# Kernel tuning notes

Measured on AMD Instinct MI355X. Metric: run time of the kernel, lower is better.

## Reference

```python
import jax, jax.numpy as jnp
import numpy as np

MARGIN = 1.0

def _safe_sqrt(x):
    # sqrt with zero gradient at x<=0 (matches relu().sqrt() forward; avoids NaN grads on the zero diagonal)
    pos = x > 0
    return jnp.where(pos, jnp.sqrt(jnp.where(pos, x, 1.0)), 0.0)

def _smoothed_metric_loss(X, m=MARGIN):
    # X: [N, d], N even; lifted-structure smoothed loss (Song et al.)
    N = X.shape[0]
    sq = jnp.sum(X * X, axis=1)                       # [N]
    G = X @ X.T                                       # [N, N]
    D = _safe_sqrt(jax.nn.relu(sq[:, None] + sq[None, :] - 2.0 * G))
    E = jnp.exp(m - D)                                # [N, N]
    P = N // 2
    i = jnp.arange(P) * 2
    j = i + 1
    # negatives for pair p: rows {i,j}, all cols except {i,j}
    row_pair_sum = E.reshape(P, 2, N).sum(axis=(1, 2))  # [P] = rowsum(i)+rowsum(j)
    excl = E[i, i] + E[i, j] + E[j, i] + E[j, j]
    neg_sum = row_pair_sum - excl
    J = jnp.log(neg_sum) + D[i, j]
    return jnp.sum(jax.nn.relu(J) ** 2) / (2.0 * P)

def reference(text_embeddings, shape_embeddings):
    N = text_embeddings.shape[0]
    # tt loss on text embeddings
    metric_tt = _smoothed_metric_loss(text_embeddings, MARGIN)
    # repeat each shape embedding twice (index_select with i//2)
    shape_rep = jnp.repeat(shape_embeddings, 2, axis=0)  # [N, d]
    mask = jnp.tile(jnp.array([1.0, 0.0], dtype=text_embeddings.dtype), N // 2)[:, None]
    inv = 1.0 - mask
    e1 = text_embeddings * mask + shape_rep * inv
    e2 = text_embeddings * inv + shape_rep * mask
    emb = jnp.concatenate([e1, e2], axis=0)              # [2N, d]
    metric_st = _smoothed_metric_loss(emb, MARGIN)
    return metric_tt + metric_st

def setup_inputs() -> dict:
    key = jax.random.key(0)
    k1, k2 = jax.random.split(key)
    N, Dim = 4096, 256
    text = jax.random.normal(k1, (N, Dim), dtype=jnp.float32)
    shape = jax.random.normal(k2, (N // 2, Dim), dtype=jnp.float32)
    return {"text_embeddings": text, "shape_embeddings": shape}
```

## Files before the change

kernel.cpp:

```cpp
#include <hip/hip_runtime.h>
#include <hip/hip_bf16.h>
#include <math.h>


typedef __bf16 bf16x8 __attribute__((ext_vector_type(8)));
typedef float floatx4 __attribute__((ext_vector_type(4)));

#define KD 256
#define NU 6144
#define NBU 48
#define TU (NBU * (NBU + 1) / 2)
#define BM 128
#define BK 32
#define ECONST 2.718281828459045f
#define LOSS_BLOCKS 1536

#define LSLOT(r, q) ((((r) * 4 + ((q) ^ (((r) >> 1) & 3)))) * 8)

__device__ __forceinline__ void gload_lds16(const void* g, void* l) {
  __builtin_amdgcn_global_load_lds((const __attribute__((address_space(1))) unsigned int*)g,
                                   (__attribute__((address_space(3))) unsigned int*)l,
                                   16, 0, 0);
}

__global__ __launch_bounds__(256) void prep_kernel(const float* __restrict__ text,
                                                   const float* __restrict__ shape,
                                                   __bf16* __restrict__ Xu,
                                                   float* __restrict__ sq,
                                                   float* __restrict__ rowacc) {
  int gt = blockIdx.x * 256 + threadIdx.x;
  if (gt < 2 * NU) rowacc[gt] = 0.f;
  int wave = gt >> 6;
  int lane = gt & 63;
  const float* src = (wave < 4096) ? (text + (size_t)wave * KD)
                                   : (shape + (size_t)(wave - 4096) * KD);
  __bf16* dst = Xu + (size_t)wave * KD;
  float s = 0.f;
#pragma unroll
  for (int j = 0; j < 4; ++j) {
    int idx = j * 64 + lane;
    float f = src[idx];
    __bf16 h = (__bf16)f;
    dst[idx] = h;
    float fv = (float)h;
    s += fv * fv;
  }
#pragma unroll
  for (int m = 1; m < 64; m <<= 1) s += __shfl_xor(s, m, 64);
  if (lane == 0) sq[wave] = s;
}

__global__ __launch_bounds__(256, 4) void egemm_tri_kernel(
    const __bf16* __restrict__ X, const float* __restrict__ sq,
    float* __restrict__ rowacc) {
  __shared__ __align__(16) __bf16 As[BM * BK];
  __shared__ __align__(16) __bf16 Bs[BM * BK];
  __shared__ float rowbuf[2][128];
  __shared__ float colbuf[2][128];

  int t = blockIdx.x;
  int by = (int)((sqrtf(8.0f * (float)t + 1.0f) - 1.0f) * 0.5f);
  while ((by + 1) * (by + 2) / 2 <= t) ++by;
  while (by * (by + 1) / 2 > t) --by;
  const int bx = t - by * (by + 1) / 2;

  const int mBase = by * BM;
  const int nBase = bx * BM;
  const bool diag = (by == bx);

  const int tid = threadIdx.x;
  const int lane = tid & 63;
  const int w = tid >> 6;
  const int warpM = w >> 1, warpN = w & 1;
  const int quad = lane >> 4;
  const int l15 = lane & 15;

  floatx4 acc[4][4] = {};

  const int sRow = lane >> 2;
  const int sCol = (((lane & 3) ^ ((lane >> 3) & 3))) * 8;

  for (int kt = 0; kt < KD; kt += BK) {
    __syncthreads();
#pragma unroll
    for (int h = 0; h < 2; ++h) {
      int c = h * 4 + w;
      gload_lds16(X + (size_t)(mBase + c * 16 + sRow) * KD + kt + sCol, &As[c * 512]);
      gload_lds16(X + (size_t)(nBase + c * 16 + sRow) * KD + kt + sCol, &Bs[c * 512]);
    }
    __syncthreads();

    bf16x8 af[4], bfr[4];
#pragma unroll
    for (int tm = 0; tm < 4; ++tm)
      af[tm] = *(const bf16x8*)&As[LSLOT(warpM * 64 + tm * 16 + l15, quad)];
#pragma unroll
    for (int tn = 0; tn < 4; ++tn)
      bfr[tn] = *(const bf16x8*)&Bs[LSLOT(warpN * 64 + tn * 16 + l15, quad)];
#pragma unroll
    for (int tm = 0; tm < 4; ++tm)
#pragma unroll
      for (int tn = 0; tn < 4; ++tn)
        acc[tm][tn] = __builtin_amdgcn_mfma_f32_16x16x32_bf16(af[tm], bfr[tn], acc[tm][tn], 0, 0, 0);
  }

  const int rbase = mBase + warpM * 64;
  const int cbase = nBase + warpN * 64;
  float sqr[4][4], sqc[4];
#pragma unroll
  for (int tm = 0; tm < 4; ++tm)
#pragma unroll
    for (int r = 0; r < 4; ++r)
      sqr[tm][r] = sq[rbase + tm * 16 + quad * 4 + r];
#pragma unroll
  for (int tn = 0; tn < 4; ++tn)
    sqc[tn] = sq[cbase + tn * 16 + l15];

  const float L2E = 1.44269504088896f;
  float cs[4] = {0.f, 0.f, 0.f, 0.f};
#pragma unroll
  for (int tm = 0; tm < 4; ++tm) {
    float rs[4] = {0.f, 0.f, 0.f, 0.f};
#pragma unroll
    for (int tn = 0; tn < 4; ++tn) {
#pragma unroll
      for (int r = 0; r < 4; ++r) {
        float v = acc[tm][tn][r];
        float dsq = fmaf(-2.0f, v, sqr[tm][r] + sqc[tn]);
        float dst = sqrtf(fmaxf(dsq, 0.f));
        float ev = __builtin_amdgcn_exp2f(fmaf(-L2E, dst, L2E));
        if (diag && tm == tn && (quad * 4 + r) == l15) ev = 0.f;
        rs[r] += ev;
        cs[tn] += ev;
      }
    }
#pragma unroll
    for (int r = 0; r < 4; ++r) {
      float v = rs[r];
      v += __shfl_xor(v, 1, 64);
      v += __shfl_xor(v, 2, 64);
      v += __shfl_xor(v, 4, 64);
      v += __shfl_xor(v, 8, 64);
      if (l15 == 0) rowbuf[warpN][warpM * 64 + tm * 16 + quad * 4 + r] = v;
    }
  }
#pragma unroll
  for (int tn = 0; tn < 4; ++tn) {
    float v = cs[tn];
    v += __shfl_xor(v, 16, 64);
    v += __shfl_xor(v, 32, 64);
    if (quad == 0) colbuf[warpM][warpN * 64 + tn * 16 + l15] = v;
  }
  __syncthreads();

  float* rdst = rowacc + (bx < 32 ? 0 : NU);
  float* cdst = rowacc + (by < 32 ? 0 : NU);
  if (tid < 128) {
    atomicAdd(&rdst[mBase + tid], rowbuf[0][tid] + rowbuf[1][tid]);
  } else if (!diag) {
    int c = tid - 128;
    atomicAdd(&cdst[nBase + c], colbuf[0][c] + colbuf[1][c]);
  }
}

__global__ __launch_bounds__(256) void loss_kernel(const float* __restrict__ text,
                                                   const float* __restrict__ shape,
                                                   const float* __restrict__ rowacc,
                                                   float* __restrict__ partials) {
  __shared__ float part[4];
  const float* St = rowacc;
  const float* Ss = rowacc + NU;
  int wv = blockIdx.x * 4 + (threadIdx.x >> 6);
  int lane = threadIdx.x & 63;
  const float *a, *b;
  float base, scale;
  if (wv < 2048) {
    int p = wv;
    a = text + (size_t)(2 * p) * KD;
    b = text + (size_t)(2 * p + 1) * KD;
    base = St[2 * p] + St[2 * p + 1];
    scale = 1.0f / 4096.0f;
  } else {
    int p = wv - 2048;
    int u1, u2;
    if (p < 2048) {
      u1 = 2 * p; u2 = 4096 + p;
      a = text + (size_t)(2 * p) * KD;
      b = shape + (size_t)p * KD;
    } else {
      int s = p - 2048;
      u1 = 4096 + s; u2 = 2 * s + 1;
      a = shape + (size_t)s * KD;
      b = text + (size_t)(2 * s + 1) * KD;
    }
    float g1 = St[u1] + 2.0f * Ss[u1];
    float g2 = St[u2] + 2.0f * Ss[u2];
    base = g1 + g2 + ECONST;
    scale = 1.0f / 8192.0f;
  }
  float s = 0.f;
#pragma unroll
  for (int j = 0; j < 4; ++j) {
    int idx = j * 64 + lane;
    float d = a[idx] - b[idx];
    s += d * d;
  }
#pragma unroll
  for (int m = 1; m < 64; m <<= 1) s += __shfl_xor(s, m, 64);
  if (lane == 0) {
    float D = s > 0.f ? sqrtf(s) : 0.f;
    float ns = base - 2.0f * expf(1.0f - D);
    float J = logf(ns) + D;
    part[threadIdx.x >> 6] = (J > 0.f) ? J * J * scale : 0.f;
  }
  __syncthreads();
  if (threadIdx.x == 0)
    partials[blockIdx.x] = part[0] + part[1] + part[2] + part[3];
}

__global__ __launch_bounds__(256) void reduce_kernel(const float* __restrict__ partials,
                                                     float* __restrict__ out, int out_n) {
  __shared__ float part[4];
  float s = 0.f;
  for (int i = threadIdx.x; i < LOSS_BLOCKS; i += 256) s += partials[i];
#pragma unroll
  for (int m = 1; m < 64; m <<= 1) s += __shfl_xor(s, m, 64);
  if ((threadIdx.x & 63) == 0) part[threadIdx.x >> 6] = s;
  __syncthreads();
  if (threadIdx.x == 0) out[0] = part[0] + part[1] + part[2] + part[3];
  else if (threadIdx.x < out_n) out[threadIdx.x] = 0.f;
}

extern "C" void kernel_launch(void* const* d_in, const int* in_sizes, int n_in,
                              void* d_out, int out_size, void* d_ws, size_t ws_size,
                              hipStream_t stream) {
  const float* text = (const float*)d_in[0];
  const float* shape = (const float*)d_in[1];
  float* out = (float*)d_out;

  char* ws = (char*)d_ws;
  __bf16* Xu = (__bf16*)ws;
  float* sq = (float*)(ws + (size_t)NU * KD * 2);
  float* rowacc = sq + NU;
  float* partials = rowacc + 2 * NU;

  prep_kernel<<<NU / 4, 256, 0, stream>>>(text, shape, Xu, sq, rowacc);
  egemm_tri_kernel<<<TU, 256, 0, stream>>>(Xu, sq, rowacc);
  loss_kernel<<<LOSS_BLOCKS, 256, 0, stream>>>(text, shape, rowacc, partials);
  reduce_kernel<<<1, 256, 0, stream>>>(partials, out, out_size);
}
```

Before: 99.21 us.

## Double-buffer GEMM LDS tiles and replace row-sum atomics with partials plus reduce kernel

Double-buffers the shared-memory A/B tiles so the next K-slice's global-to-LDS load is issued before the current slice's MFMAs, with one barrier per iteration instead of two. Also replaces per-tile atomicAdd into row accumulators with plain per-tile partial writes, summed by a new deterministic rowreduce kernel. This removes atomic contention and the zeroing pass in prep. In exchange it uses twice the LDS per block, adds a kernel launch, and the reduce kernel runs only 24 blocks, each looping over up to 48 partials serially.

```diff
diff --git a/kernel.cpp b/kernel.cpp
--- a/kernel.cpp
+++ b/kernel.cpp
@@ -26,10 +26,8 @@
 __global__ __launch_bounds__(256) void prep_kernel(const float* __restrict__ text,
                                                    const float* __restrict__ shape,
                                                    __bf16* __restrict__ Xu,
-                                                   float* __restrict__ sq,
-                                                   float* __restrict__ rowacc) {
+                                                   float* __restrict__ sq) {
   int gt = blockIdx.x * 256 + threadIdx.x;
-  if (gt < 2 * NU) rowacc[gt] = 0.f;
   int wave = gt >> 6;
   int lane = gt & 63;
   const float* src = (wave < 4096) ? (text + (size_t)wave * KD)
@@ -52,13 +50,13 @@
 
 __global__ __launch_bounds__(256, 4) void egemm_tri_kernel(
     const __bf16* __restrict__ X, const float* __restrict__ sq,
-    float* __restrict__ rowacc) {
-  __shared__ __align__(16) __bf16 As[BM * BK];
-  __shared__ __align__(16) __bf16 Bs[BM * BK];
+    float* __restrict__ rowpart, float* __restrict__ colpart) {
+  __shared__ __align__(16) __bf16 As[2][BM * BK];
+  __shared__ __align__(16) __bf16 Bs[2][BM * BK];
   __shared__ float rowbuf[2][128];
   __shared__ float colbuf[2][128];
 
-  int t = blockIdx.x;
+  const int t = blockIdx.x;
   int by = (int)((sqrtf(8.0f * (float)t + 1.0f) - 1.0f) * 0.5f);
   while ((by + 1) * (by + 2) / 2 <= t) ++by;
   while (by * (by + 1) / 2 > t) --by;
@@ -80,28 +78,35 @@
   const int sRow = lane >> 2;
   const int sCol = (((lane & 3) ^ ((lane >> 3) & 3))) * 8;
 
-  for (int kt = 0; kt < KD; kt += BK) {
-    __syncthreads();
-#pragma unroll
-    for (int h = 0; h < 2; ++h) {
-      int c = h * 4 + w;
-      gload_lds16(X + (size_t)(mBase + c * 16 + sRow) * KD + kt + sCol, &As[c * 512]);
-      gload_lds16(X + (size_t)(nBase + c * 16 + sRow) * KD + kt + sCol, &Bs[c * 512]);
-    }
-    __syncthreads();
+#define STAGE(buf, kt)                                                                     \
+  {                                                                                        \
+    _Pragma("unroll") for (int h = 0; h < 2; ++h) {                                        \
+      int c = h * 4 + w;                                                                   \
+      gload_lds16(X + (size_t)(mBase + c * 16 + sRow) * KD + (kt) + sCol, &As[buf][c * 512]); \
+      gload_lds16(X + (size_t)(nBase + c * 16 + sRow) * KD + (kt) + sCol, &Bs[buf][c * 512]); \
+    }                                                                                      \
+  }
+
+  STAGE(0, 0);
+  __syncthreads();
+#pragma unroll
+  for (int i = 0; i < KD / BK; ++i) {
+    const int cur = i & 1;
+    if (i < KD / BK - 1) STAGE(cur ^ 1, (i + 1) * BK);
 
     bf16x8 af[4], bfr[4];
 #pragma unroll
     for (int tm = 0; tm < 4; ++tm)
-      af[tm] = *(const bf16x8*)&As[LSLOT(warpM * 64 + tm * 16 + l15, quad)];
+      af[tm] = *(const bf16x8*)&As[cur][LSLOT(warpM * 64 + tm * 16 + l15, quad)];
 #pragma unroll
     for (int tn = 0; tn < 4; ++tn)
-      bfr[tn] = *(const bf16x8*)&Bs[LSLOT(warpN * 64 + tn * 16 + l15, quad)];
+      bfr[tn] = *(const bf16x8*)&Bs[cur][LSLOT(warpN * 64 + tn * 16 + l15, quad)];
 #pragma unroll
     for (int tm = 0; tm < 4; ++tm)
 #pragma unroll
       for (int tn = 0; tn < 4; ++tn)
         acc[tm][tn] = __builtin_amdgcn_mfma_f32_16x16x32_bf16(af[tm], bfr[tn], acc[tm][tn], 0, 0, 0);
+    __syncthreads();
   }
 
   const int rbase = mBase + warpM * 64;
@@ -153,14 +158,31 @@
   }
   __syncthreads();
 
-  float* rdst = rowacc + (bx < 32 ? 0 : NU);
-  float* cdst = rowacc + (by < 32 ? 0 : NU);
   if (tid < 128) {
-    atomicAdd(&rdst[mBase + tid], rowbuf[0][tid] + rowbuf[1][tid]);
-  } else if (!diag) {
+    rowpart[(size_t)t * 128 + tid] = rowbuf[0][tid] + rowbuf[1][tid];
+  } else {
     int c = tid - 128;
-    atomicAdd(&cdst[nBase + c], colbuf[0][c] + colbuf[1][c]);
-  }
+    colpart[(size_t)t * 128 + c] = diag ? 0.f : (colbuf[0][c] + colbuf[1][c]);
+  }
+}
+
+__global__ __launch_bounds__(256) void rowreduce_kernel(const float* __restrict__ rowpart,
+                                                        const float* __restrict__ colpart,
+                                                        float* __restrict__ rowacc) {
+  const int s = blockIdx.x * 2 + (threadIdx.x >> 7);
+  const int r = threadIdx.x & 127;
+  float stv = 0.f, ssv = 0.f;
+  const int base = s * (s + 1) / 2;
+  for (int bx = 0; bx <= s; ++bx) {
+    float v = rowpart[(size_t)(base + bx) * 128 + r];
+    if (bx < 32) stv += v; else ssv += v;
+  }
+  for (int by = s + 1; by < NBU; ++by) {
+    float v = colpart[(size_t)(by * (by + 1) / 2 + s) * 128 + r];
+    if (by < 32) stv += v; else ssv += v;
+  }
+  rowacc[s * 128 + r] = stv;
+  rowacc[NU + s * 128 + r] = ssv;
 }
 
 __global__ __launch_bounds__(256) void loss_kernel(const float* __restrict__ text,
@@ -243,9 +265,12 @@
   float* sq = (float*)(ws + (size_t)NU * KD * 2);
   float* rowacc = sq + NU;
   float* partials = rowacc + 2 * NU;
-
-  prep_kernel<<<NU / 4, 256, 0, stream>>>(text, shape, Xu, sq, rowacc);
-  egemm_tri_kernel<<<TU, 256, 0, stream>>>(Xu, sq, rowacc);
+  float* rowpart = partials + LOSS_BLOCKS;
+  float* colpart = rowpart + (size_t)TU * 128;
+
+  prep_kernel<<<NU / 4, 256, 0, stream>>>(text, shape, Xu, sq);
+  egemm_tri_kernel<<<TU, 256, 0, stream>>>(Xu, sq, rowpart, colpart);
+  rowreduce_kernel<<<NBU / 2, 256, 0, stream>>>(rowpart, colpart, rowacc);
   loss_kernel<<<LOSS_BLOCKS, 256, 0, stream>>>(text, shape, rowacc, partials);
   reduce_kernel<<<1, 256, 0, stream>>>(partials, out, out_size);
 }
```

Result: slower. 113.3 us (+14.2%).
